# Performance work log

Measured on AMD Instinct MI355X. Metric: run time of the kernel, lower is better.

Reference implementation:

```python
import jax, jax.numpy as jnp
import numpy as np

N_CLASSES = 43
G = 4            # n_grid
N_ITER = 3
EPS = 1e-5


def _conv(x, w, b, stride, pad):
    y = jax.lax.conv_general_dilated(
        x, w, (stride, stride), [(pad, pad), (pad, pad)],
        dimension_numbers=("NCHW", "OIHW", "NCHW"))
    return y + b[None, :, None, None]


def _bn(x, gamma, beta):
    # training-mode batch norm (batch statistics, biased variance)
    m = jnp.mean(x, axis=(0, 2, 3), keepdims=True)
    v = jnp.mean((x - m) ** 2, axis=(0, 2, 3), keepdims=True)
    xh = (x - m) * jax.lax.rsqrt(v + EPS)
    return xh * gamma[None, :, None, None] + beta[None, :, None, None]


def _lrelu(x):
    return jnp.where(x >= 0, x, 0.1 * x)


def _squash(v):
    sn = jnp.sum(v * v, axis=-1, keepdims=True)
    return (sn / (1.0 + sn)) * v / jnp.sqrt(sn)


def setup_inputs() -> dict:
    key = jax.random.key(0)
    ks = jax.random.split(key, 24)
    f32 = jnp.float32
    d = {}
    d["x"] = jax.random.normal(ks[0], (8, 3, 128, 128), dtype=f32)
    # conv backbone params (He-ish scale)
    def w(k, shape, fan_in):
        return jax.random.normal(k, shape, dtype=f32) * (1.0 / np.sqrt(fan_in))
    d["c1w"] = w(ks[1], (128, 3, 3, 3), 3 * 9);   d["c1b"] = jnp.zeros((128,), f32)
    d["g1"] = jnp.ones((128,), f32);              d["b1"] = jnp.zeros((128,), f32)
    d["c2w"] = w(ks[2], (256, 128, 3, 3), 128 * 9); d["c2b"] = jnp.zeros((256,), f32)
    d["g2"] = jnp.ones((256,), f32);              d["b2"] = jnp.zeros((256,), f32)
    d["c3w"] = w(ks[3], (64, 256, 4, 4), 256 * 16); d["c3b"] = jnp.zeros((64,), f32)
    d["g3"] = jnp.ones((64,), f32);               d["b3"] = jnp.zeros((64,), f32)
    d["c4w"] = w(ks[4], (128, 64, 4, 4), 64 * 16);  d["c4b"] = jnp.zeros((128,), f32)
    d["g4"] = jnp.ones((128,), f32);              d["b4"] = jnp.zeros((128,), f32)
    d["c5w"] = w(ks[5], (256, 128, 4, 4), 128 * 16); d["c5b"] = jnp.zeros((256,), f32)
    d["g5"] = jnp.ones((256,), f32);              d["b5"] = jnp.zeros((256,), f32)
    # route weights: torch shape (1, n_nodes, n_caps, in_C, out_C); drop leading 1
    d["rw"] = 0.1 * jax.random.normal(ks[6], (512, N_CLASSES, 8, 21), dtype=f32)
    return d


def reference(x, c1w, c1b, g1, b1, c2w, c2b, g2, b2, c3w, c3b, g3, b3,
              c4w, c4b, g4, b4, c5w, c5b, g5, b5, rw):
    B = x.shape[0]
    h = _lrelu(_bn(_conv(x, c1w, c1b, 1, 1), g1, b1))
    h = _lrelu(_bn(_conv(h, c2w, c2b, 1, 1), g2, b2))
    h = _lrelu(_bn(_conv(h, c3w, c3b, 2, 1), g3, b3))
    h = _lrelu(_bn(_conv(h, c4w, c4b, 2, 1), g4, b4))
    h = _lrelu(_bn(_conv(h, c5w, c5b, 2, 1), g5, b5))  # [B,256,4G,4G]
    # view(B,256,4,4*G^2) -> chunk G^2 along last -> per chunk permute(0,2,3,1).view(B,512,8), stack chunks first
    y = h.reshape(B, 256, 4, G * G, 4)                # (B,C,h,chunk,w)
    y = jnp.transpose(y, (3, 0, 2, 4, 1))             # (G^2,B,h,w,C)
    caps_in = y.reshape(G * G * B, 512, 8)            # B' = G^2*B
    # priors: [B',n_nodes,n_caps,out_C]
    priors = jnp.einsum("bni,nkio->bnko", caps_in, rw)
    logits = jnp.zeros_like(priors)
    outputs = None
    for i in range(N_ITER):
        probs = jax.nn.softmax(logits, axis=2)
        s = jnp.sum(probs * priors, axis=1, keepdims=True)  # [B',1,k,21]
        outputs = _squash(s)
        if i != N_ITER - 1:
            logits = logits + jnp.sum(priors * outputs, axis=-1, keepdims=True)
    out = outputs[:, 0]                               # [B',k,21]
    out = out.reshape(G, G, B, N_CLASSES, 21)
    return jnp.transpose(out, (2, 0, 1, 3, 4))        # [B,G,G,k,21]
```

## Files before the change

kernel.cpp:

```cpp
#include <hip/hip_runtime.h>
#include <math.h>

typedef unsigned int   uint;
typedef unsigned short ushort;
using bf16x8 = __attribute__((ext_vector_type(8))) __bf16;
using f32x4  = __attribute__((ext_vector_type(4))) float;

constexpr int NB   = 128;
constexpr int NCAP = 512;
constexpr int NCLS = 43;
constexpr int NO   = 21;
constexpr int KO   = NCLS * NO;

constexpr size_t F_X1H  = 0;
constexpr size_t F_X1L  = 8388608;
constexpr size_t F_PART = 0;
constexpr size_t F_STAT = 16777216;
constexpr size_t F_WPH  = 16778240;
constexpr size_t F_WPL  = 16925696;
constexpr size_t F_W3H  = 17073152;
constexpr size_t F_W3L  = 17204224;
constexpr size_t F_W4H  = 17335296;
constexpr size_t F_W4L  = 17400832;
constexpr size_t F_W5H  = 17466368;
constexpr size_t F_W5L  = 17728512;
constexpr size_t F_X3H  = 17990656;
constexpr size_t F_X3L  = 34767872;
constexpr size_t F_H3   = 51545088;
constexpr size_t F_X4H  = 53642240;
constexpr size_t F_X4L  = 54690816;
constexpr size_t F_H4   = 55739392;
constexpr size_t F_X5H  = 56787968;
constexpr size_t F_X5L  = 57312256;
constexpr size_t F_H5   = 57836544;
constexpr size_t F_PRI  = 0;
constexpr size_t F_CAPS = 59179008;
constexpr size_t F_LOG  = 59703296;
constexpr size_t F_S    = 65339392;
constexpr size_t F_OUTS = 65454976;
constexpr size_t F_ZERO = 65570560;

__device__ inline ushort f2bf(float x) {
  uint u = __float_as_uint(x);
  uint r = (u + 0x7fffu + ((u >> 16) & 1u)) >> 16;
  return (ushort)r;
}
__device__ inline float bf2f(ushort h) { return __uint_as_float(((uint)h) << 16); }

#define GLL16(gsrc, ldst)                                               \
  __builtin_amdgcn_global_load_lds(                                     \
      (const __attribute__((address_space(1))) void*)(gsrc),            \
      (__attribute__((address_space(3))) void*)(ldst), 16, 0, 0)

__global__ __launch_bounds__(256) void conv1_k(
    const float* __restrict__ in, const float* __restrict__ w,
    ushort* __restrict__ oh, ushort* __restrict__ ol,
    float* __restrict__ stats)
{
  constexpr int KS = 3, ICC = 3, IHT = 10, IWT = 18;
  const int ocb = blockIdx.z & 3;
  const int b   = blockIdx.z >> 2;
  const int tx0 = blockIdx.x * 16;
  const int ty0 = blockIdx.y * 8;
  const int oc0 = ocb * 32;

  __shared__ float lin[ICC][IHT][IWT];
  __shared__ float lw[ICC][KS * KS][32];
  __shared__ float b1sum[32], b1sq[32];

  const int t  = threadIdx.x;
  const int pq = t & 3;
  const int ty = (t >> 2) & 7;
  const int oq = t >> 5;

  float acc[4][4];
#pragma unroll
  for (int m = 0; m < 4; ++m)
#pragma unroll
    for (int j = 0; j < 4; ++j) acc[m][j] = 0.f;

  const int gx0 = tx0 - 1;
  const int gy0 = ty0 - 1;

  for (int e = t; e < ICC * IHT * IWT; e += 256) {
    int ic = e / (IHT * IWT);
    int rr = e % (IHT * IWT);
    int ey = rr / IWT, ex = rr % IWT;
    int gy = gy0 + ey, gx = gx0 + ex;
    float v = 0.f;
    if ((unsigned)gy < 128u && (unsigned)gx < 128u)
      v = in[((size_t)(b * 3 + ic) * 128 + gy) * 128 + gx];
    lin[ic][ey][ex] = v;
  }
  for (int e = t; e < ICC * 9 * 32; e += 256) {
    int ocl = e & 31;
    int rr  = e >> 5;
    int kk  = rr % 9;
    int ic  = rr / 9;
    lw[ic][kk][ocl] = w[((size_t)(oc0 + ocl) * 3 + ic) * 9 + kk];
  }
  __syncthreads();

  for (int ic = 0; ic < ICC; ++ic) {
#pragma unroll
    for (int ky = 0; ky < KS; ++ky) {
#pragma unroll
      for (int kx = 0; kx < KS; ++kx) {
        float xv[4];
#pragma unroll
        for (int j = 0; j < 4; ++j)
          xv[j] = lin[ic][ty + ky][pq * 4 + j + kx];
        const float4 w4 = *(const float4*)&lw[ic][ky * KS + kx][oq * 4];
#pragma unroll
        for (int j = 0; j < 4; ++j) {
          acc[0][j] = fmaf(w4.x, xv[j], acc[0][j]);
          acc[1][j] = fmaf(w4.y, xv[j], acc[1][j]);
          acc[2][j] = fmaf(w4.z, xv[j], acc[2][j]);
          acc[3][j] = fmaf(w4.w, xv[j], acc[3][j]);
        }
      }
    }
  }

  const int oy = ty0 + ty;
  const int oc0q = oc0 + oq * 4;
  const size_t icb = oc0q >> 3;
  const int off = oc0q & 7;
  float sm[4] = {0.f, 0.f, 0.f, 0.f}, qm[4] = {0.f, 0.f, 0.f, 0.f};
#pragma unroll
  for (int j = 0; j < 4; ++j) {
    int px = tx0 + pq * 4 + j;
    size_t pxg = ((size_t)b * 128 + oy) * 128 + px;
    size_t addr = (icb * 131072 + pxg) * 8 + off;
    ushort h0 = f2bf(acc[0][j]); ushort l0 = f2bf(acc[0][j] - bf2f(h0));
    ushort h1 = f2bf(acc[1][j]); ushort l1 = f2bf(acc[1][j] - bf2f(h1));
    ushort h2 = f2bf(acc[2][j]); ushort l2 = f2bf(acc[2][j] - bf2f(h2));
    ushort h3 = f2bf(acc[3][j]); ushort l3 = f2bf(acc[3][j] - bf2f(h3));
    uint2 uh; uh.x = (uint)h0 | ((uint)h1 << 16); uh.y = (uint)h2 | ((uint)h3 << 16);
    uint2 ul; ul.x = (uint)l0 | ((uint)l1 << 16); ul.y = (uint)l2 | ((uint)l3 << 16);
    *(uint2*)(oh + addr) = uh;
    *(uint2*)(ol + addr) = ul;
    float v0 = bf2f(h0) + bf2f(l0), v1 = bf2f(h1) + bf2f(l1);
    float v2 = bf2f(h2) + bf2f(l2), v3 = bf2f(h3) + bf2f(l3);
    sm[0] += v0; qm[0] += v0 * v0;
    sm[1] += v1; qm[1] += v1 * v1;
    sm[2] += v2; qm[2] += v2 * v2;
    sm[3] += v3; qm[3] += v3 * v3;
  }
#pragma unroll
  for (int o = 16; o > 0; o >>= 1) {
#pragma unroll
    for (int m = 0; m < 4; ++m) {
      sm[m] += __shfl_xor(sm[m], o);
      qm[m] += __shfl_xor(qm[m], o);
    }
  }
  if ((t & 31) == 0) {
#pragma unroll
    for (int m = 0; m < 4; ++m) { b1sum[oq * 4 + m] = sm[m]; b1sq[oq * 4 + m] = qm[m]; }
  }
  __syncthreads();
  if (t < 32) {
    atomicAdd(&stats[oc0 + t], b1sum[t]);
    atomicAdd(&stats[128 + oc0 + t], b1sq[t]);
  }
}

__global__ __launch_bounds__(256) void bn_apply_x1_k(
    ushort* __restrict__ xh, ushort* __restrict__ xl,
    const float* __restrict__ stats, const float* __restrict__ g,
    const float* __restrict__ bt)
{
  __shared__ float scs[128], sfs[128];
  const int t = threadIdx.x;
  if (t < 128) {
    float m = stats[t] * (1.f / 131072.f);
    float v = stats[128 + t] * (1.f / 131072.f) - m * m;
    float rs = rsqrtf(v + 1e-5f);
    float sc = g[t] * rs;
    scs[t] = sc; sfs[t] = bt[t] - m * sc;
  }
  __syncthreads();
  const size_t total = (size_t)16 * 131072;
  const size_t stride = (size_t)gridDim.x * 256;
  for (size_t i = (size_t)blockIdx.x * 256 + t; i < total; i += stride) {
    int j = (int)(i >> 17);
    int c0 = j * 8;
    uint4 vh = *(const uint4*)(xh + i * 8);
    uint4 vl = *(const uint4*)(xl + i * 8);
    uint hw[4] = {vh.x, vh.y, vh.z, vh.w};
    uint lw[4] = {vl.x, vl.y, vl.z, vl.w};
    uint ohv[4], olv[4];
#pragma unroll
    for (int m = 0; m < 4; ++m) {
      float f0 = __uint_as_float(hw[m] << 16) + __uint_as_float(lw[m] << 16);
      float f1 = __uint_as_float(hw[m] & 0xffff0000u) + __uint_as_float(lw[m] & 0xffff0000u);
      float a0 = fmaf(f0, scs[c0 + 2*m],   sfs[c0 + 2*m]);   a0 = fmaxf(a0, 0.1f * a0);
      float a1 = fmaf(f1, scs[c0 + 2*m+1], sfs[c0 + 2*m+1]); a1 = fmaxf(a1, 0.1f * a1);
      ushort h0 = f2bf(a0), l0 = f2bf(a0 - bf2f(h0));
      ushort h1 = f2bf(a1), l1 = f2bf(a1 - bf2f(h1));
      ohv[m] = (uint)h0 | ((uint)h1 << 16);
      olv[m] = (uint)l0 | ((uint)l1 << 16);
    }
    uint4 rh = {ohv[0], ohv[1], ohv[2], ohv[3]};
    uint4 rl = {olv[0], olv[1], olv[2], olv[3]};
    *(uint4*)(xh + i * 8) = rh;
    *(uint4*)(xl + i * 8) = rl;
  }
}

__global__ __launch_bounds__(256) void bn_stats_nhwc_k(
    const float* __restrict__ x, float* __restrict__ stats,
    int cmask, int lg2c, int totpx)
{
  int g = blockIdx.x * 256 + threadIdx.x;
  int c = g & cmask;
  int p0 = g >> lg2c;
  int stride = (gridDim.x * 256) >> lg2c;
  float s = 0.f, q = 0.f;
  for (int p = p0; p < totpx; p += stride) {
    float v = x[((size_t)p << lg2c) | c];
    s += v; q += v * v;
  }
  atomicAdd(&stats[c], s);
  atomicAdd(&stats[cmask + 1 + c], q);
}

template<int C>
__global__ __launch_bounds__(256) void split_blocked_k(
    const float* __restrict__ h, const float* __restrict__ stats,
    const float* __restrict__ g, const float* __restrict__ bt, float inv_n,
    ushort* __restrict__ oh, ushort* __restrict__ ol, int totpx)
{
  __shared__ ushort lh[16][C + 8], ll[16][C + 8];
  __shared__ float scs[C], sfs[C];
  const int px0 = blockIdx.x * 16;
  const int t = threadIdx.x;
  if (t < C) {
    float m = stats[t] * inv_n;
    float v = stats[C + t] * inv_n - m * m;
    float rs = rsqrtf(v + 1e-5f);
    float sc = g[t] * rs;
    scs[t] = sc; sfs[t] = bt[t] - m * sc;
  }
  __syncthreads();
  for (int e = t; e < 16 * C / 4; e += 256) {
    int px = e / (C / 4);
    int c0 = (e % (C / 4)) * 4;
    float4 v  = *(const float4*)(h + (size_t)(px0 + px) * C + c0);
    float a0 = fmaf(v.x, scs[c0],   sfs[c0]);   a0 = fmaxf(a0, 0.1f * a0);
    float a1 = fmaf(v.y, scs[c0+1], sfs[c0+1]); a1 = fmaxf(a1, 0.1f * a1);
    float a2 = fmaf(v.z, scs[c0+2], sfs[c0+2]); a2 = fmaxf(a2, 0.1f * a2);
    float a3 = fmaf(v.w, scs[c0+3], sfs[c0+3]); a3 = fmaxf(a3, 0.1f * a3);
    ushort h0 = f2bf(a0), h1 = f2bf(a1), h2v = f2bf(a2), h3v = f2bf(a3);
    lh[px][c0]   = h0;  ll[px][c0]   = f2bf(a0 - bf2f(h0));
    lh[px][c0+1] = h1;  ll[px][c0+1] = f2bf(a1 - bf2f(h1));
    lh[px][c0+2] = h2v; ll[px][c0+2] = f2bf(a2 - bf2f(h2v));
    lh[px][c0+3] = h3v; ll[px][c0+3] = f2bf(a3 - bf2f(h3v));
  }
  __syncthreads();
  for (int e = t; e < 16 * (C / 8); e += 256) {
    int j = e >> 4, px = e & 15;
    *(uint4*)(oh + ((size_t)j * totpx + px0 + px) * 8) = *(const uint4*)&lh[px][j * 8];
    *(uint4*)(ol + ((size_t)j * totpx + px0 + px) * 8) = *(const uint4*)&ll[px][j * 8];
  }
}

__global__ void wsplit_all_k(
    const float* __restrict__ c2w, const float* __restrict__ c3w,
    const float* __restrict__ c4w, const float* __restrict__ c5w,
    ushort* __restrict__ wph, ushort* __restrict__ wpl,
    ushort* __restrict__ w3h, ushort* __restrict__ w3l,
    ushort* __restrict__ w4h, ushort* __restrict__ w4l,
    ushort* __restrict__ w5h, ushort* __restrict__ w5l)
{
  int i = blockIdx.x * 256 + threadIdx.x;
  if (i < 294912) {
    int kk = i % 9; int r = i / 9; int ic = r & 127; int oc = r >> 7;
    float v = c2w[i];
    ushort hi = f2bf(v), lo = f2bf(v - bf2f(hi));
    int ohf = oc >> 7, of = (oc >> 4) & 7, lr = oc & 15;
    int ic32 = ic >> 5, kg = (ic >> 3) & 3, ici = ic & 7;
    size_t d = ((((size_t)(kk * 4 + ic32) * 2 + ohf) * 8 + of) * 4 + kg) * 128
               + lr * 8 + ici;
    wph[d] = hi; wpl[d] = lo;
    return;
  }
  i -= 294912;
  const float* w; ushort *wh, *wl; int OC, IC, n;
  if (i < 262144)      { w = c3w; wh = w3h; wl = w3l; OC = 64;  IC = 256; n = i; }
  else if (i < 393216) { w = c4w; wh = w4h; wl = w4l; OC = 128; IC = 64;  n = i - 262144; }
  else if (i < 917504) { w = c5w; wh = w5h; wl = w5l; OC = 256; IC = 128; n = i - 393216; }
  else return;
  int kx = n & 3, ky = (n >> 2) & 3;
  int ic = (n >> 4) % IC, oc = (n >> 4) / IC;
  float v = w[n];
  ushort hi = f2bf(v), lo = f2bf(v - bf2f(hi));
  int NCH = IC >> 3, NWO = OC >> 6;
  int wo = oc >> 6, of = (oc >> 4) & 3, lr = oc & 15;
  int ch = ic >> 3, ici = ic & 7;
  size_t d = ((((size_t)(ky * NCH + ch) * NWO + wo) * 4 + of) * 4 + kx) * 128
             + lr * 8 + ici;
  wh[d] = hi; wl[d] = lo;
}

__device__ __forceinline__ void stage_x(
    const ushort* __restrict__ x1h, const ushort* __restrict__ x1l,
    const ushort* __restrict__ zbuf,
    ushort* xh_dst, ushort* xl_dst, int t, int b, int gy, int ic32)
{
  const bool rowok = (unsigned)gy < 128u;
  const size_t rowb = ((size_t)b * 128 + (rowok ? gy : 0)) * 128;
#pragma unroll
  for (int k = 0; k < 2; ++k) {
    int e = t + k * 256;
    int icg = e / 130;
    int xi = e - icg * 130;
    int gx = xi - 1;
    const ushort* sh = zbuf;
    const ushort* sl = zbuf;
    if (rowok && (unsigned)gx < 128u) {
      size_t gi = ((size_t)(ic32 * 4 + icg) * 131072 + rowb + gx) * 8;
      sh = x1h + gi; sl = x1l + gi;
    }
    GLL16(sh, xh_dst + (size_t)e * 8);
    GLL16(sl, xl_dst + (size_t)e * 8);
  }
  if (t < 8) {
    int e = 512 + t;
    int xi = e - 390;
    int gx = xi - 1;
    const ushort* sh = zbuf;
    const ushort* sl = zbuf;
    if (rowok && (unsigned)gx < 128u) {
      size_t gi = ((size_t)(ic32 * 4 + 3) * 131072 + rowb + gx) * 8;
      sh = x1h + gi; sl = x1l + gi;
    }
    GLL16(sh, xh_dst + (size_t)e * 8);
    GLL16(sl, xl_dst + (size_t)e * 8);
  }
}

__global__ __launch_bounds__(256, 2) void conv2_mfma_k(
    const ushort* __restrict__ x1h, const ushort* __restrict__ x1l,
    const ushort* __restrict__ wph, const ushort* __restrict__ wpl,
    const ushort* __restrict__ zbuf, float* __restrict__ stats2,
    ushort* __restrict__ x3h, ushort* __restrict__ x3l)
{
  const int bid = blockIdx.x;
  const int wid = (bid & 7) * 128 + (bid >> 3);
  const int y0  = wid & 127;
  const int b   = wid >> 7;

  __shared__ ushort xs[2][2][4][130][8];
  __shared__ float bsum[2][256], bsq[2][256];

  const int t = threadIdx.x;
  const int w  = t >> 6;
  const int l  = t & 63;
  const int xhf = w & 1;
  const int ohf = w >> 1;
  const int lr = l & 15;
  const int kg = l >> 4;

  f32x4 acc[8][4];
#pragma unroll
  for (int i = 0; i < 8; ++i)
#pragma unroll
    for (int j = 0; j < 4; ++j) acc[i][j] = (f32x4){0.f, 0.f, 0.f, 0.f};

  stage_x(x1h, x1l, zbuf, (ushort*)&xs[0][0][0][0][0], (ushort*)&xs[0][1][0][0][0],
          t, b, y0 - 1, 0);
  __syncthreads();

  for (int ky = 0; ky < 3; ++ky) {
    for (int ic32 = 0; ic32 < 4; ++ic32) {
      const int buf = ic32 & 1;
      const int np = ky * 4 + ic32 + 1;
      if (np < 12) {
        const int nbuf = buf ^ 1;
        stage_x(x1h, x1l, zbuf,
                (ushort*)&xs[nbuf][0][0][0][0], (ushort*)&xs[nbuf][1][0][0][0],
                t, b, y0 + (np >> 2) - 1, np & 3);
      }
#pragma unroll
      for (int kx = 0; kx < 3; ++kx) {
        const int kk = ky * 3 + kx;
        const size_t wbase =
            ((size_t)((kk * 4 + ic32) * 2 + ohf)) * 4096 + (size_t)l * 8;
        const ushort* pwh = wph + wbase;
        const ushort* pwl = wpl + wbase;

        bf16x8 xbh[4], xbl[4];
#pragma unroll
        for (int pf = 0; pf < 4; ++pf) {
          int xi = xhf * 64 + pf * 16 + lr + kx;
          xbh[pf] = *(const bf16x8*)&xs[buf][0][kg][xi][0];
          xbl[pf] = *(const bf16x8*)&xs[buf][1][kg][xi][0];
        }
#pragma unroll
        for (int oh2 = 0; oh2 < 2; ++oh2) {
          bf16x8 awh[4], awl[4];
#pragma unroll
          for (int o4 = 0; o4 < 4; ++o4) {
            awh[o4] = *(const bf16x8*)(pwh + (oh2 * 4 + o4) * 512);
            awl[o4] = *(const bf16x8*)(pwl + (oh2 * 4 + o4) * 512);
          }
#pragma unroll
          for (int o4 = 0; o4 < 4; ++o4) {
            const int of = oh2 * 4 + o4;
#pragma unroll
            for (int pf = 0; pf < 4; ++pf) {
              acc[of][pf] = __builtin_amdgcn_mfma_f32_16x16x32_bf16(awh[o4], xbh[pf], acc[of][pf], 0, 0, 0);
              acc[of][pf] = __builtin_amdgcn_mfma_f32_16x16x32_bf16(awh[o4], xbl[pf], acc[of][pf], 0, 0, 0);
              acc[of][pf] = __builtin_amdgcn_mfma_f32_16x16x32_bf16(awl[o4], xbh[pf], acc[of][pf], 0, 0, 0);
            }
          }
        }
      }
      __syncthreads();
    }
  }

#pragma unroll
  for (int of = 0; of < 8; ++of) {
    float s4[4] = {0.f, 0.f, 0.f, 0.f}, q4[4] = {0.f, 0.f, 0.f, 0.f};
#pragma unroll
    for (int pf = 0; pf < 4; ++pf) {
      int oc = ohf * 128 + of * 16 + kg * 4;
      int x  = xhf * 64 + pf * 16 + lr;
      size_t pxg = ((size_t)b * 128 + y0) * 128 + x;
      size_t base = ((size_t)(oc >> 3) * 131072 + pxg) * 8 + (oc & 7);
      f32x4 a = acc[of][pf];
      ushort h0 = f2bf(a[0]); ushort l0 = f2bf(a[0] - bf2f(h0));
      ushort h1 = f2bf(a[1]); ushort l1 = f2bf(a[1] - bf2f(h1));
      ushort h2 = f2bf(a[2]); ushort l2 = f2bf(a[2] - bf2f(h2));
      ushort h3 = f2bf(a[3]); ushort l3 = f2bf(a[3] - bf2f(h3));
      uint2 uh; uh.x = (uint)h0 | ((uint)h1 << 16); uh.y = (uint)h2 | ((uint)h3 << 16);
      uint2 ul; ul.x = (uint)l0 | ((uint)l1 << 16); ul.y = (uint)l2 | ((uint)l3 << 16);
      *(uint2*)(x3h + base) = uh;
      *(uint2*)(x3l + base) = ul;
      float v0 = bf2f(h0) + bf2f(l0), v1 = bf2f(h1) + bf2f(l1);
      float v2 = bf2f(h2) + bf2f(l2), v3 = bf2f(h3) + bf2f(l3);
      s4[0] += v0; q4[0] += v0 * v0;
      s4[1] += v1; q4[1] += v1 * v1;
      s4[2] += v2; q4[2] += v2 * v2;
      s4[3] += v3; q4[3] += v3 * v3;
    }
#pragma unroll
    for (int o = 8; o > 0; o >>= 1) {
#pragma unroll
      for (int j = 0; j < 4; ++j) {
        s4[j] += __shfl_xor(s4[j], o);
        q4[j] += __shfl_xor(q4[j], o);
      }
    }
    if (lr == 0) {
      int oc = ohf * 128 + of * 16 + kg * 4;
#pragma unroll
      for (int j = 0; j < 4; ++j) { bsum[xhf][oc + j] = s4[j]; bsq[xhf][oc + j] = q4[j]; }
    }
  }
  __syncthreads();
  if (t < 256) {
    atomicAdd(&stats2[t],       bsum[0][t] + bsum[1][t]);
    atomicAdd(&stats2[256 + t], bsq[0][t] + bsq[1][t]);
  }
}

template<int IC, int OC, int OH, int OW, int WPX, int CS, bool FBN>
__global__ __launch_bounds__(256, 2) void convs_mfma_k(
    const ushort* __restrict__ xh, const ushort* __restrict__ xl,
    const ushort* __restrict__ wh, const ushort* __restrict__ wl,
    const float* __restrict__ stats, const float* __restrict__ gg,
    const float* __restrict__ bb, float inv_n,
    float* __restrict__ part)
{
  constexpr int IH  = 2 * OH, IW = 2 * OW;
  constexpr int NCH = IC / 8;
  constexpr int NCHB = NCH / CS;
  constexpr int PFX = OW / 16;
  constexpr int RW  = 4 / WPX;
  constexpr int NZ = 4 * CS;
  constexpr int NX = OH / 4;
  constexpr int NWO = OC / 64;
  constexpr int SBN = FBN ? IC : 1;

  const int bid = blockIdx.x;
  const int wid = (bid & 7) * (NZ * NX) + (bid >> 3);
  const int zi = wid % NZ;
  const int y0 = ((wid / NZ) % NX) * 4;
  const int b  = wid / (NZ * NX);
  const int ky = zi & 3;
  const int cs = zi >> 2;

  __shared__ ushort xs[2][4][2][OW + 2][8];
  __shared__ float scs[SBN], sfs[SBN];

  const int t = threadIdx.x;
  if (FBN) {
    for (int c = t; c < IC; c += 256) {
      float m = stats[c] * inv_n;
      float v = stats[IC + c] * inv_n - m * m;
      float rs = rsqrtf(v + 1e-5f);
      float sc = gg[c] * rs;
      scs[c] = sc; sfs[c] = bb[c] - m * sc;
    }
  }

  const int w = t >> 6, l = t & 63;
  const int wo = w / WPX, wp = w % WPX;
  const int lr = l & 15, kg = l >> 4;
  const int oc0w = wo * 64;
  const int rb = wp * RW;

  f32x4 acc[4][4];
#pragma unroll
  for (int i = 0; i < 4; ++i)
#pragma unroll
    for (int j = 0; j < 4; ++j) acc[i][j] = (f32x4){0.f, 0.f, 0.f, 0.f};

  for (int cc = 0; cc < NCHB; ++cc) {
    const int ch = cs * NCHB + cc;
    __syncthreads();
    for (int e = t; e < 4 * (IW + 2); e += 256) {
      int r  = e / (IW + 2);
      int xi = e % (IW + 2);
      int xp = xi - 1;
      int iy = 2 * (y0 + r) + ky - 1;
      uint4 rh = {0, 0, 0, 0}, rl = {0, 0, 0, 0};
      if ((unsigned)iy < (unsigned)IH && (unsigned)xp < (unsigned)IW) {
        size_t gi = ((((size_t)ch * 8 + b) * IH + iy) * IW + xp) * 8;
        uint4 vh = *(const uint4*)(xh + gi);
        uint4 vl = *(const uint4*)(xl + gi);
        if (FBN) {
          int c0 = ch * 8;
          uint hw[4] = {vh.x, vh.y, vh.z, vh.w};
          uint lw[4] = {vl.x, vl.y, vl.z, vl.w};
          uint ohv[4], olv[4];
#pragma unroll
          for (int m = 0; m < 4; ++m) {
            float f0 = __uint_as_float(hw[m] << 16) + __uint_as_float(lw[m] << 16);
            float f1 = __uint_as_float(hw[m] & 0xffff0000u) + __uint_as_float(lw[m] & 0xffff0000u);
            float a0 = fmaf(f0, scs[c0 + 2*m],   sfs[c0 + 2*m]);   a0 = fmaxf(a0, 0.1f * a0);
            float a1 = fmaf(f1, scs[c0 + 2*m+1], sfs[c0 + 2*m+1]); a1 = fmaxf(a1, 0.1f * a1);
            ushort h0 = f2bf(a0), l0 = f2bf(a0 - bf2f(h0));
            ushort h1 = f2bf(a1), l1 = f2bf(a1 - bf2f(h1));
            ohv[m] = (uint)h0 | ((uint)h1 << 16);
            olv[m] = (uint)l0 | ((uint)l1 << 16);
          }
          rh.x = ohv[0]; rh.y = ohv[1]; rh.z = ohv[2]; rh.w = ohv[3];
          rl.x = olv[0]; rl.y = olv[1]; rl.z = olv[2]; rl.w = olv[3];
        } else {
          rh = vh; rl = vl;
        }
      }
      int par = xp & 1;
      int idx = (xp + 1) >> 1;
      *(uint4*)&xs[0][r][par][idx][0] = rh;
      *(uint4*)&xs[1][r][par][idx][0] = rl;
    }
    __syncthreads();

    const size_t wbase =
        ((size_t)(ky * NCH + ch) * NWO + wo) * 2048 + (size_t)l * 8;
    bf16x8 ah[4], al[4], bh[4], bl[4];
#pragma unroll
    for (int of = 0; of < 4; ++of) {
      ah[of] = *(const bf16x8*)(wh + wbase + of * 512);
      al[of] = *(const bf16x8*)(wl + wbase + of * 512);
    }
    const int par = 1 - (kg & 1);
    const int xoff = kg >> 1;
#pragma unroll
    for (int pf = 0; pf < 4; ++pf) {
      int row = rb + pf / PFX;
      int x   = (pf % PFX) * 16 + lr;
      bh[pf] = *(const bf16x8*)&xs[0][row][par][x + xoff][0];
      bl[pf] = *(const bf16x8*)&xs[1][row][par][x + xoff][0];
    }
#pragma unroll
    for (int of = 0; of < 4; ++of) {
#pragma unroll
      for (int pf = 0; pf < 4; ++pf) {
        acc[of][pf] = __builtin_amdgcn_mfma_f32_16x16x32_bf16(ah[of], bh[pf], acc[of][pf], 0, 0, 0);
        acc[of][pf] = __builtin_amdgcn_mfma_f32_16x16x32_bf16(ah[of], bl[pf], acc[of][pf], 0, 0, 0);
        acc[of][pf] = __builtin_amdgcn_mfma_f32_16x16x32_bf16(al[of], bh[pf], acc[of][pf], 0, 0, 0);
      }
    }
  }

  float* yp = part + (size_t)zi * (8 * OH * OW * OC);
#pragma unroll
  for (int of = 0; of < 4; ++of) {
#pragma unroll
    for (int pf = 0; pf < 4; ++pf) {
      int row = rb + pf / PFX;
      int x   = (pf % PFX) * 16 + lr;
      int oc  = oc0w + of * 16 + kg * 4;
      float* p = yp + (((size_t)b * OH + y0 + row) * OW + x) * OC + oc;
      f32x4 a = acc[of][pf];
      float4 v = {a[0], a[1], a[2], a[3]};
      *(float4*)p = v;
    }
  }
}

__global__ __launch_bounds__(256) void reduce_k(
    const float* __restrict__ part, float* __restrict__ h,
    int n4, int nparts)
{
  int i = blockIdx.x * 256 + threadIdx.x;
  if (i >= n4) return;
  float4 a = ((const float4*)part)[i];
  for (int z = 1; z < nparts; ++z) {
    float4 b = ((const float4*)part)[(size_t)z * n4 + i];
    a.x += b.x; a.y += b.y; a.z += b.z; a.w += b.w;
  }
  ((float4*)h)[i] = a;
}

__global__ void caps_k(const float* __restrict__ h5, const float* __restrict__ stats,
                       const float* __restrict__ g5, const float* __restrict__ b5,
                       float* __restrict__ caps)
{
  int e = blockIdx.x * 256 + threadIdx.x;
  if (e >= NB * NCAP * 8) return;
  int ii = e & 7;
  int n  = (e >> 3) & 511;
  int jb = e >> 12;
  int j = jb >> 3, b = jb & 7;
  int i = n >> 7, k = (n >> 5) & 3, ch = ((n & 31) << 3) | ii;
  int hh = (i << 2) | (j >> 2);
  int ww = ((j & 3) << 2) | k;
  float m  = stats[ch] * (1.f / 2048.f);
  float vv = stats[256 + ch] * (1.f / 2048.f) - m * m;
  float rs = rsqrtf(vv + 1e-5f);
  float sc = g5[ch] * rs;
  float sf = b5[ch] - m * sc;
  float v = h5[(((size_t)b * 16 + hh) * 16 + ww) * 256 + ch];
  float a = fmaf(v, sc, sf);
  a = fmaxf(a, 0.1f * a);
  caps[e] = a;
}

__global__ __launch_bounds__(256) void priors_k(
    const float* __restrict__ caps, const float* __restrict__ rw,
    ushort* __restrict__ priors)
{
  const int n = blockIdx.x;
  __shared__ float lrw[NCLS * 8 * NO];
  __shared__ float lc[NB * 8];
  const int t = threadIdx.x;
  for (int e = t; e < NCLS * 8 * NO; e += 256)
    lrw[e] = rw[(size_t)n * NCLS * 8 * NO + e];
  for (int e = t; e < NB * 8; e += 256) {
    int b = e >> 3, ii = e & 7;
    lc[e] = caps[((size_t)b * NCAP + n) * 8 + ii];
  }
  __syncthreads();

  int p[4], kk[4], oo[4];
#pragma unroll
  for (int q = 0; q < 4; ++q) {
    p[q]  = t + q * 256;
    kk[q] = (p[q] < KO) ? p[q] / NO : 0;
    oo[q] = (p[q] < KO) ? p[q] % NO : 0;
  }
  for (int b = 0; b < NB; ++b) {
    const float* cb = &lc[b * 8];
    float c0 = cb[0], c1 = cb[1], c2 = cb[2], c3 = cb[3];
    float c4 = cb[4], c5 = cb[5], c6 = cb[6], c7 = cb[7];
    ushort* pout = priors + ((size_t)b * NCAP + n) * KO;
#pragma unroll
    for (int q = 0; q < 4; ++q) {
      if (p[q] < KO) {
        const float* wv = &lrw[kk[q] * (8 * NO) + oo[q]];
        float a = c0 * wv[0];
        a = fmaf(c1, wv[21],  a);
        a = fmaf(c2, wv[42],  a);
        a = fmaf(c3, wv[63],  a);
        a = fmaf(c4, wv[84],  a);
        a = fmaf(c5, wv[105], a);
        a = fmaf(c6, wv[126], a);
        a = fmaf(c7, wv[147], a);
        pout[p[q]] = f2bf(a);
      }
    }
  }
}

__global__ __launch_bounds__(256) void route_s_partial(
    const ushort* __restrict__ priors, float* __restrict__ s)
{
  const int b  = blockIdx.x >> 3;
  const int ns = blockIdx.x & 7;
  const int t  = threadIdx.x;
  const int p0 = t, p1 = t + 256, p2 = t + 512, p3 = t + 768;
  float a0 = 0.f, a1 = 0.f, a2 = 0.f, a3 = 0.f;
  const ushort* pb = priors + ((size_t)b * NCAP + ns * 64) * KO;
#pragma unroll 2
  for (int n = 0; n < 64; ++n) {
    const ushort* pn = pb + (size_t)n * KO;
    a0 += bf2f(pn[p0]); a1 += bf2f(pn[p1]); a2 += bf2f(pn[p2]);
    if (p3 < KO) a3 += bf2f(pn[p3]);
  }
  const float sc = 1.f / 43.f;
  atomicAdd(&s[b * KO + p0], a0 * sc);
  atomicAdd(&s[b * KO + p1], a1 * sc);
  atomicAdd(&s[b * KO + p2], a2 * sc);
  if (p3 < KO) atomicAdd(&s[b * KO + p3], a3 * sc);
}

__global__ __launch_bounds__(256) void route_iter_k(
    const ushort* __restrict__ priors, const float* __restrict__ souts,
    float* __restrict__ logits, float* __restrict__ s,
    int readPrev, int writeL)
{
  const int b  = blockIdx.x >> 3;
  const int ns = blockIdx.x & 7;
  const int t  = threadIdx.x;
  const int w  = t >> 6;
  const int lane = t & 63;

  __shared__ float so_l[KO];
  __shared__ float sacc[4][KO];
  __shared__ float prow[4][KO];
  __shared__ float pk[4][NCLS];

  for (int e = t; e < KO; e += 256) so_l[e] = souts[b * KO + e];
  for (int e = lane; e < KO; e += 64) sacc[w][e] = 0.f;

  int kq[15];
#pragma unroll
  for (int q = 0; q < 15; ++q) {
    int e = lane + q * 64;
    kq[q] = (e < KO) ? e / NO : 0;
  }
  __syncthreads();

  for (int nn = 0; nn < 16; ++nn) {
    const int n = ns * 64 + w * 16 + nn;
    const ushort* pr = priors + ((size_t)(b * NCAP + n)) * KO;
    float v[15];
#pragma unroll
    for (int q = 0; q < 15; ++q) {
      int e = lane + q * 64;
      if (e < KO) { v[q] = bf2f(pr[e]); prow[w][e] = v[q]; }
      else v[q] = 0.f;
    }
    __syncthreads();

    float L = -1e30f;
    if (lane < NCLS) {
      float d = 0.f;
      const float* pp = &prow[w][lane * NO];
      const float* ss = &so_l[lane * NO];
#pragma unroll
      for (int o = 0; o < NO; ++o) d = fmaf(pp[o], ss[o], d);
      size_t lidx = ((size_t)(b * NCAP + n)) * NCLS + lane;
      L = (readPrev ? logits[lidx] : 0.f) + d;
      if (writeL) logits[lidx] = L;
    }
    float m = L;
#pragma unroll
    for (int off = 32; off > 0; off >>= 1) m = fmaxf(m, __shfl_xor(m, off));
    float ex = (lane < NCLS) ? __expf(L - m) : 0.f;
    float sm = ex;
#pragma unroll
    for (int off = 32; off > 0; off >>= 1) sm += __shfl_xor(sm, off);
    if (lane < NCLS) pk[w][lane] = ex / sm;
    __syncthreads();

#pragma unroll
    for (int q = 0; q < 15; ++q) {
      int e = lane + q * 64;
      if (e < KO) sacc[w][e] += pk[w][kq[q]] * v[q];
    }
  }
  __syncthreads();
  for (int e = t; e < KO; e += 256)
    atomicAdd(&s[b * KO + e], sacc[0][e] + sacc[1][e] + sacc[2][e] + sacc[3][e]);
}

__global__ void squash_k(const float* __restrict__ s, float* __restrict__ souts)
{
  int i = blockIdx.x * 256 + threadIdx.x;
  if (i >= NB * NCLS) return;
  int b = i / NCLS, k = i % NCLS;
  const float* sv = s + b * KO + k * NO;
  float sn = 0.f;
#pragma unroll
  for (int o = 0; o < NO; ++o) sn += sv[o] * sv[o];
  float f = sqrtf(sn) / (1.f + sn);
  float* ov = souts + b * KO + k * NO;
#pragma unroll
  for (int o = 0; o < NO; ++o) ov[o] = sv[o] * f;
}

__global__ void out_k(const float* __restrict__ souts, float* __restrict__ out)
{
  int i = blockIdx.x * 256 + threadIdx.x;
  if (i >= 8 * 16 * NCLS * NO) return;
  int o = i % NO;
  int r = i / NO;
  int k = r % NCLS; r /= NCLS;
  int g1 = r & 3; r >>= 2;
  int g0 = r & 3;
  int b  = r >> 2;
  int j  = g0 * 4 + g1;
  int jb = j * 8 + b;
  out[i] = souts[jb * KO + k * NO + o];
}

extern "C" void kernel_launch(void* const* d_in, const int* in_sizes, int n_in,
                              void* d_out, int out_size, void* d_ws, size_t ws_size,
                              hipStream_t stream)
{
  const float* x   = (const float*)d_in[0];
  const float* c1w = (const float*)d_in[1];
  const float* g1  = (const float*)d_in[3];  const float* b1  = (const float*)d_in[4];
  const float* c2w = (const float*)d_in[5];
  const float* g2  = (const float*)d_in[7];  const float* b2  = (const float*)d_in[8];
  const float* c3w = (const float*)d_in[9];
  const float* g3  = (const float*)d_in[11]; const float* b3  = (const float*)d_in[12];
  const float* c4w = (const float*)d_in[13];
  const float* g4  = (const float*)d_in[15]; const float* b4  = (const float*)d_in[16];
  const float* c5w = (const float*)d_in[17];
  const float* g5  = (const float*)d_in[19]; const float* b5  = (const float*)d_in[20];
  const float* rw  = (const float*)d_in[21];

  float* ws  = (float*)d_ws;
  float* out = (float*)d_out;

  ushort* x1h = (ushort*)(ws + F_X1H);
  ushort* x1l = (ushort*)(ws + F_X1L);
  ushort* wph = (ushort*)(ws + F_WPH);
  ushort* wpl = (ushort*)(ws + F_WPL);
  ushort* w3h = (ushort*)(ws + F_W3H);
  ushort* w3l = (ushort*)(ws + F_W3L);
  ushort* w4h = (ushort*)(ws + F_W4H);
  ushort* w4l = (ushort*)(ws + F_W4L);
  ushort* w5h = (ushort*)(ws + F_W5H);
  ushort* w5l = (ushort*)(ws + F_W5L);
  ushort* x3h = (ushort*)(ws + F_X3H);
  ushort* x3l = (ushort*)(ws + F_X3L);
  ushort* x4h = (ushort*)(ws + F_X4H);
  ushort* x4l = (ushort*)(ws + F_X4L);
  ushort* x5h = (ushort*)(ws + F_X5H);
  ushort* x5l = (ushort*)(ws + F_X5L);
  float* part   = ws + F_PART;
  float* h3     = ws + F_H3;
  float* h4     = ws + F_H4;
  float* h5     = ws + F_H5;
  float* caps   = ws + F_CAPS;
  ushort* priors = (ushort*)(ws + F_PRI);
  float* logits = ws + F_LOG;
  float* sbuf   = ws + F_S;
  float* souts  = ws + F_OUTS;
  float* stats  = ws + F_STAT;
  float* stats2 = ws + F_STAT + 512;
  ushort* zbuf  = (ushort*)(ws + F_ZERO);

  hipMemsetAsync(stats, 0, 1024 * sizeof(float), stream);
  hipMemsetAsync(zbuf, 0, 64, stream);

  wsplit_all_k<<<(1212416 + 255) / 256, 256, 0, stream>>>(
      c2w, c3w, c4w, c5w, wph, wpl, w3h, w3l, w4h, w4l, w5h, w5l);

  conv1_k<<<dim3(8, 16, 32), 256, 0, stream>>>(x, c1w, x1h, x1l, stats);

  bn_apply_x1_k<<<2048, 256, 0, stream>>>(x1h, x1l, stats, g1, b1);

  conv2_mfma_k<<<1024, 256, 0, stream>>>(x1h, x1l, wph, wpl, zbuf, stats2, x3h, x3l);

  convs_mfma_k<256, 64, 64, 64, 4, 1, true><<<512, 256, 0, stream>>>(
      x3h, x3l, w3h, w3l, stats2, g2, b2, 1.f / 131072.f, part);
  reduce_k<<<(524288 + 255) / 256, 256, 0, stream>>>(part, h3, 524288, 4);
  hipMemsetAsync(stats, 0, 2 * 64 * sizeof(float), stream);
  bn_stats_nhwc_k<<<256, 256, 0, stream>>>(h3, stats, 63, 6, 32768);
  split_blocked_k<64><<<2048, 256, 0, stream>>>(h3, stats, g3, b3, 1.f / 32768.f, x4h, x4l, 32768);

  convs_mfma_k<64, 128, 32, 32, 2, 2, false><<<512, 256, 0, stream>>>(
      x4h, x4l, w4h, w4l, stats, g4, b4, 0.f, part);
  reduce_k<<<(262144 + 255) / 256, 256, 0, stream>>>(part, h4, 262144, 8);
  hipMemsetAsync(stats, 0, 2 * 128 * sizeof(float), stream);
  bn_stats_nhwc_k<<<128, 256, 0, stream>>>(h4, stats, 127, 7, 8192);
  split_blocked_k<128><<<512, 256, 0, stream>>>(h4, stats, g4, b4, 1.f / 8192.f, x5h, x5l, 8192);

  convs_mfma_k<128, 256, 16, 16, 1, 2, false><<<256, 256, 0, stream>>>(
      x5h, x5l, w5h, w5l, stats, g5, b5, 0.f, part);
  reduce_k<<<(131072 + 255) / 256, 256, 0, stream>>>(part, h5, 131072, 8);
  hipMemsetAsync(stats, 0, 2 * 256 * sizeof(float), stream);
  bn_stats_nhwc_k<<<64, 256, 0, stream>>>(h5, stats, 255, 8, 2048);

  caps_k<<<2048, 256, 0, stream>>>(h5, stats, g5, b5, caps);
  priors_k<<<512, 256, 0, stream>>>(caps, rw, priors);

  hipMemsetAsync(sbuf, 0, NB * KO * sizeof(float), stream);
  route_s_partial<<<NB * 8, 256, 0, stream>>>(priors, sbuf);
  squash_k<<<(NB * NCLS + 255) / 256, 256, 0, stream>>>(sbuf, souts);

  hipMemsetAsync(sbuf, 0, NB * KO * sizeof(float), stream);
  route_iter_k<<<NB * 8, 256, 0, stream>>>(priors, souts, logits, sbuf, 0, 1);
  squash_k<<<(NB * NCLS + 255) / 256, 256, 0, stream>>>(sbuf, souts);

  hipMemsetAsync(sbuf, 0, NB * KO * sizeof(float), stream);
  route_iter_k<<<NB * 8, 256, 0, stream>>>(priors, souts, logits, sbuf, 1, 0);
  squash_k<<<(NB * NCLS + 255) / 256, 256, 0, stream>>>(sbuf, souts);

  out_k<<<(8 * 16 * NCLS * NO + 255) / 256, 256, 0, stream>>>(souts, out);
}
```

Baseline: 702.6 us.

## Triple-buffer conv2 input staging and register-resident routing accumulation

The conv2 kernel now stages input rows into a three-deep LDS ring, prefetching two stages ahead. It uses explicit vmcnt waits and a single barrier per stage, replacing double buffering with two syncs. The routing iteration kernel keeps per-class prior slices, squashed outputs and accumulators in registers per lane. This removes the per-node block-wide barriers and shared-memory scatter of probabilities. The changes add LDS usage and register pressure, and rely on intra-wave ordering for the shared prow staging.

```diff
diff --git a/kernel.cpp b/kernel.cpp
--- a/kernel.cpp
+++ b/kernel.cpp
@@ -304,10 +304,10 @@
   wh[d] = hi; wl[d] = lo;
 }
 
-__device__ __forceinline__ void stage_x(
+__device__ __forceinline__ void stage_x3(
     const ushort* __restrict__ x1h, const ushort* __restrict__ x1l,
     const ushort* __restrict__ zbuf,
-    ushort* xh_dst, ushort* xl_dst, int t, int b, int gy, int ic32)
+    ushort* xh_dst, ushort* xl_dst, int t, int b, int gy)
 {
   const bool rowok = (unsigned)gy < 128u;
   const size_t rowb = ((size_t)b * 128 + (rowok ? gy : 0)) * 128;
@@ -315,29 +315,32 @@
   for (int k = 0; k < 2; ++k) {
     int e = t + k * 256;
     int icg = e / 130;
-    int xi = e - icg * 130;
-    int gx = xi - 1;
+    int xi  = e - icg * 130;
+    int gx  = xi - 1;
     const ushort* sh = zbuf;
     const ushort* sl = zbuf;
     if (rowok && (unsigned)gx < 128u) {
-      size_t gi = ((size_t)(ic32 * 4 + icg) * 131072 + rowb + gx) * 8;
+      size_t gi = ((size_t)icg * 131072 + rowb + gx) * 8;
       sh = x1h + gi; sl = x1l + gi;
     }
     GLL16(sh, xh_dst + (size_t)e * 8);
     GLL16(sl, xl_dst + (size_t)e * 8);
   }
-  if (t < 8) {
-    int e = 512 + t;
+  {
+    int wv = t >> 6, lane = t & 63;
+    int e  = 512 + wv * 2 + lane;
     int xi = e - 390;
     int gx = xi - 1;
-    const ushort* sh = zbuf;
-    const ushort* sl = zbuf;
-    if (rowok && (unsigned)gx < 128u) {
-      size_t gi = ((size_t)(ic32 * 4 + 3) * 131072 + rowb + gx) * 8;
-      sh = x1h + gi; sl = x1l + gi;
-    }
-    GLL16(sh, xh_dst + (size_t)e * 8);
-    GLL16(sl, xl_dst + (size_t)e * 8);
+    if (lane < 2) {
+      const ushort* sh = zbuf;
+      const ushort* sl = zbuf;
+      if (rowok && (unsigned)gx < 128u) {
+        size_t gi = ((size_t)3 * 131072 + rowb + gx) * 8;
+        sh = x1h + gi; sl = x1l + gi;
+      }
+      GLL16(sh, xh_dst + (size_t)e * 8);
+      GLL16(sl, xl_dst + (size_t)e * 8);
+    }
   }
 }
 
@@ -352,7 +355,7 @@
   const int y0  = wid & 127;
   const int b   = wid >> 7;
 
-  __shared__ ushort xs[2][2][4][130][8];
+  __shared__ ushort xs[3][2][4][130][8];
   __shared__ float bsum[2][256], bsq[2][256];
 
   const int t = threadIdx.x;
@@ -369,56 +372,66 @@
 #pragma unroll
     for (int j = 0; j < 4; ++j) acc[i][j] = (f32x4){0.f, 0.f, 0.f, 0.f};
 
-  stage_x(x1h, x1l, zbuf, (ushort*)&xs[0][0][0][0][0], (ushort*)&xs[0][1][0][0][0],
-          t, b, y0 - 1, 0);
-  __syncthreads();
-
-  for (int ky = 0; ky < 3; ++ky) {
-    for (int ic32 = 0; ic32 < 4; ++ic32) {
-      const int buf = ic32 & 1;
-      const int np = ky * 4 + ic32 + 1;
-      if (np < 12) {
-        const int nbuf = buf ^ 1;
-        stage_x(x1h, x1l, zbuf,
-                (ushort*)&xs[nbuf][0][0][0][0], (ushort*)&xs[nbuf][1][0][0][0],
-                t, b, y0 + (np >> 2) - 1, np & 3);
+  stage_x3(x1h + (size_t)(0 * 4) * 131072 * 8, x1l + (size_t)(0 * 4) * 131072 * 8,
+           zbuf, (ushort*)&xs[0][0][0][0][0], (ushort*)&xs[0][1][0][0][0],
+           t, b, y0 - 1);
+  stage_x3(x1h + (size_t)(1 * 4) * 131072 * 8, x1l + (size_t)(1 * 4) * 131072 * 8,
+           zbuf, (ushort*)&xs[1][0][0][0][0], (ushort*)&xs[1][1][0][0][0],
+           t, b, y0 - 1);
+
+  for (int p = 0; p < 12; ++p) {
+    if (p < 11) { asm volatile("s_waitcnt vmcnt(6)" ::: "memory"); }
+    else        { asm volatile("s_waitcnt vmcnt(0)" ::: "memory"); }
+    __builtin_amdgcn_sched_barrier(0);
+    __builtin_amdgcn_s_barrier();
+    __builtin_amdgcn_sched_barrier(0);
+
+    if (p + 2 < 12) {
+      const int np = p + 2;
+      stage_x3(x1h + (size_t)((np & 3) * 4) * 131072 * 8,
+               x1l + (size_t)((np & 3) * 4) * 131072 * 8,
+               zbuf,
+               (ushort*)&xs[np % 3][0][0][0][0], (ushort*)&xs[np % 3][1][0][0][0],
+               t, b, y0 + (np >> 2) - 1);
+    }
+
+    const int buf  = p % 3;
+    const int ky   = p >> 2;
+    const int ic32 = p & 3;
+#pragma unroll
+    for (int kx = 0; kx < 3; ++kx) {
+      const int kk = ky * 3 + kx;
+      const size_t wbase =
+          ((size_t)((kk * 4 + ic32) * 2 + ohf)) * 4096 + (size_t)l * 8;
+      const ushort* pwh = wph + wbase;
+      const ushort* pwl = wpl + wbase;
+
+      bf16x8 xbh[4], xbl[4];
+#pragma unroll
+      for (int pf = 0; pf < 4; ++pf) {
+        int xi = xhf * 64 + pf * 16 + lr + kx;
+        xbh[pf] = *(const bf16x8*)&xs[buf][0][kg][xi][0];
+        xbl[pf] = *(const bf16x8*)&xs[buf][1][kg][xi][0];
       }
 #pragma unroll
-      for (int kx = 0; kx < 3; ++kx) {
-        const int kk = ky * 3 + kx;
-        const size_t wbase =
-            ((size_t)((kk * 4 + ic32) * 2 + ohf)) * 4096 + (size_t)l * 8;
-        const ushort* pwh = wph + wbase;
-        const ushort* pwl = wpl + wbase;
-
-        bf16x8 xbh[4], xbl[4];
-#pragma unroll
-        for (int pf = 0; pf < 4; ++pf) {
-          int xi = xhf * 64 + pf * 16 + lr + kx;
-          xbh[pf] = *(const bf16x8*)&xs[buf][0][kg][xi][0];
-          xbl[pf] = *(const bf16x8*)&xs[buf][1][kg][xi][0];
+      for (int oh2 = 0; oh2 < 2; ++oh2) {
+        bf16x8 awh[4], awl[4];
+#pragma unroll
+        for (int o4 = 0; o4 < 4; ++o4) {
+          awh[o4] = *(const bf16x8*)(pwh + (oh2 * 4 + o4) * 512);
+          awl[o4] = *(const bf16x8*)(pwl + (oh2 * 4 + o4) * 512);
         }
 #pragma unroll
-        for (int oh2 = 0; oh2 < 2; ++oh2) {
-          bf16x8 awh[4], awl[4];
-#pragma unroll
-          for (int o4 = 0; o4 < 4; ++o4) {
-            awh[o4] = *(const bf16x8*)(pwh + (oh2 * 4 + o4) * 512);
-            awl[o4] = *(const bf16x8*)(pwl + (oh2 * 4 + o4) * 512);
-          }
-#pragma unroll
-          for (int o4 = 0; o4 < 4; ++o4) {
-            const int of = oh2 * 4 + o4;
-#pragma unroll
-            for (int pf = 0; pf < 4; ++pf) {
-              acc[of][pf] = __builtin_amdgcn_mfma_f32_16x16x32_bf16(awh[o4], xbh[pf], acc[of][pf], 0, 0, 0);
-              acc[of][pf] = __builtin_amdgcn_mfma_f32_16x16x32_bf16(awh[o4], xbl[pf], acc[of][pf], 0, 0, 0);
-              acc[of][pf] = __builtin_amdgcn_mfma_f32_16x16x32_bf16(awl[o4], xbh[pf], acc[of][pf], 0, 0, 0);
-            }
+        for (int o4 = 0; o4 < 4; ++o4) {
+          const int of = oh2 * 4 + o4;
+#pragma unroll
+          for (int pf = 0; pf < 4; ++pf) {
+            acc[of][pf] = __builtin_amdgcn_mfma_f32_16x16x32_bf16(awh[o4], xbh[pf], acc[of][pf], 0, 0, 0);
+            acc[of][pf] = __builtin_amdgcn_mfma_f32_16x16x32_bf16(awh[o4], xbl[pf], acc[of][pf], 0, 0, 0);
+            acc[of][pf] = __builtin_amdgcn_mfma_f32_16x16x32_bf16(awl[o4], xbh[pf], acc[of][pf], 0, 0, 0);
           }
         }
       }
-      __syncthreads();
     }
   }
 
@@ -722,42 +735,33 @@
   const int t  = threadIdx.x;
   const int w  = t >> 6;
   const int lane = t & 63;
-
-  __shared__ float so_l[KO];
-  __shared__ float sacc[4][KO];
-  __shared__ float prow[4][KO];
-  __shared__ float pk[4][NCLS];
-
-  for (int e = t; e < KO; e += 256) so_l[e] = souts[b * KO + e];
-  for (int e = lane; e < KO; e += 64) sacc[w][e] = 0.f;
-
-  int kq[15];
-#pragma unroll
-  for (int q = 0; q < 15; ++q) {
-    int e = lane + q * 64;
-    kq[q] = (e < KO) ? e / NO : 0;
-  }
-  __syncthreads();
+  const bool act = lane < NCLS;
+
+  __shared__ float prow[4][928];
+
+  float so[NO], sacc[NO], v[NO];
+  if (act) {
+#pragma unroll
+    for (int o = 0; o < NO; ++o) so[o] = souts[b * KO + lane * NO + o];
+  }
+#pragma unroll
+  for (int o = 0; o < NO; ++o) { sacc[o] = 0.f; v[o] = 0.f; }
 
   for (int nn = 0; nn < 16; ++nn) {
     const int n = ns * 64 + w * 16 + nn;
     const ushort* pr = priors + ((size_t)(b * NCAP + n)) * KO;
-    float v[15];
 #pragma unroll
     for (int q = 0; q < 15; ++q) {
       int e = lane + q * 64;
-      if (e < KO) { v[q] = bf2f(pr[e]); prow[w][e] = v[q]; }
-      else v[q] = 0.f;
-    }
-    __syncthreads();
-
+      if (e < KO) prow[w][e] = bf2f(pr[e]);
+    }
     float L = -1e30f;
-    if (lane < NCLS) {
+    if (act) {
       float d = 0.f;
-      const float* pp = &prow[w][lane * NO];
-      const float* ss = &so_l[lane * NO];
-#pragma unroll
-      for (int o = 0; o < NO; ++o) d = fmaf(pp[o], ss[o], d);
+#pragma unroll
+      for (int o = 0; o < NO; ++o) v[o] = prow[w][lane * NO + o];
+#pragma unroll
+      for (int o = 0; o < NO; ++o) d = fmaf(v[o], so[o], d);
       size_t lidx = ((size_t)(b * NCAP + n)) * NCLS + lane;
       L = (readPrev ? logits[lidx] : 0.f) + d;
       if (writeL) logits[lidx] = L;
@@ -765,22 +769,23 @@
     float m = L;
 #pragma unroll
     for (int off = 32; off > 0; off >>= 1) m = fmaxf(m, __shfl_xor(m, off));
-    float ex = (lane < NCLS) ? __expf(L - m) : 0.f;
+    float ex = act ? __expf(L - m) : 0.f;
     float sm = ex;
 #pragma unroll
     for (int off = 32; off > 0; off >>= 1) sm += __shfl_xor(sm, off);
-    if (lane < NCLS) pk[w][lane] = ex / sm;
-    __syncthreads();
-
-#pragma unroll
-    for (int q = 0; q < 15; ++q) {
-      int e = lane + q * 64;
-      if (e < KO) sacc[w][e] += pk[w][kq[q]] * v[q];
-    }
+    float pk = ex / sm;
+    if (act) {
+#pragma unroll
+      for (int o = 0; o < NO; ++o) sacc[o] = fmaf(pk, v[o], sacc[o]);
+    }
+  }
+  if (act) {
+#pragma unroll
+    for (int o = 0; o < NO; ++o) prow[w][lane * NO + o] = sacc[o];
   }
   __syncthreads();
   for (int e = t; e < KO; e += 256)
-    atomicAdd(&s[b * KO + e], sacc[0][e] + sacc[1][e] + sacc[2][e] + sacc[3][e]);
+    atomicAdd(&s[b * KO + e], prow[0][e] + prow[1][e] + prow[2][e] + prow[3][e]);
 }
 
 __global__ void squash_k(const float* __restrict__ s, float* __restrict__ souts)
```

After: 681.1 us. 1.03x faster.
